# Optimization experiments

Measured on AMD Instinct MI355X. Metric: run time of the kernel, lower is better.

The kernel has to match this reference:

```python
import jax, jax.numpy as jnp
import numpy as np

B, S, D, H = 2, 2048, 1024, 16
HD = D // H  # head_dim = 64


def setup_inputs() -> dict:
    key = jax.random.key(0)
    ks = jax.random.split(key, 12)
    s = 1.0 / np.sqrt(D)
    return {
        "query": jax.random.normal(ks[0], (B, S, D), jnp.float32),
        "key": jax.random.normal(ks[1], (B, S, D), jnp.float32),
        "value": jax.random.normal(ks[2], (B, S, D), jnp.float32),
        "attention_mask": jnp.zeros((B, S, S), jnp.float32),
        "WQ_w": jax.random.normal(ks[3], (D, D), jnp.float32) * s,
        "WQ_b": jnp.zeros((D,), jnp.float32),
        "WK_w": jax.random.normal(ks[4], (D, D), jnp.float32) * s,
        "WK_b": jnp.zeros((D,), jnp.float32),
        "WV_w": jax.random.normal(ks[5], (D, D), jnp.float32) * s,
        "WV_b": jnp.zeros((D,), jnp.float32),
        "WO_w": jax.random.normal(ks[6], (D, D), jnp.float32) * s,
        "WO_b": jnp.zeros((D,), jnp.float32),
    }


def _split_heads(x):
    # [B,S,D] -> [B,H,S,HD]
    b, s, _ = x.shape
    return x.reshape(b, s, H, HD).transpose(0, 2, 1, 3)


def reference(query, key, value, attention_mask,
              WQ_w, WQ_b, WK_w, WK_b, WV_w, WV_b, WO_w, WO_b):
    Q = _split_heads(query @ WQ_w.T + WQ_b)   # [B,H,S,HD]
    K = _split_heads(key @ WK_w.T + WK_b)
    V = _split_heads(value @ WV_w.T + WV_b)
    scale = 1.0 / jnp.sqrt(jnp.float32(HD))
    scores = jnp.einsum('bhqd,bhkd->bhqk', Q, K) * scale
    scores = scores + attention_mask[:, None, :, :]
    attn = jax.nn.softmax(scores, axis=-1)    # dropout_prob=0.0 -> identity
    out = jnp.einsum('bhqk,bhkd->bhqd', attn, V)
    out = out.transpose(0, 2, 1, 3).reshape(query.shape[0], -1, D)
    return out @ WO_w.T + WO_b
```

## Files before the change

kernel.cpp:

```cpp
#include <hip/hip_runtime.h>
#include <math.h>


typedef _Float16 h8 __attribute__((ext_vector_type(8)));
typedef _Float16 h4 __attribute__((ext_vector_type(4)));
typedef float f4 __attribute__((ext_vector_type(4)));

#define MFMA16(a, b, c) __builtin_amdgcn_mfma_f32_16x16x32_f16((a), (b), (c), 0, 0, 0)
#define EXP2F(x) __builtin_amdgcn_exp2f(x)
#define BARRIER_LDS() asm volatile("s_waitcnt lgkmcnt(0)\n\ts_barrier" ::: "memory")

static constexpr int Bn = 2, Sn = 2048, Dn = 1024, Hn = 16, HDn = 64;
static constexpr int Mn = Bn * Sn;
static constexpr int Kn = Dn;
static constexpr int Nn = Dn;
static constexpr int LDP = 72;
static constexpr float LOG2E = 1.4426950408889634f;

__device__ __forceinline__ void gload_lds16(const _Float16* g, _Float16* l) {
  __builtin_amdgcn_global_load_lds(
      (const __attribute__((address_space(1))) unsigned int*)g,
      (__attribute__((address_space(3))) unsigned int*)l, 16, 0, 0);
}

struct CvtJobs {
  const float* src[8];
  _Float16* dst[8];
  int n4[8];
  float scl[8];
};

__global__ __launch_bounds__(256) void cvt_kernel(CvtJobs j) {
  const int stride = gridDim.x * blockDim.x;
  const int t0 = blockIdx.x * blockDim.x + threadIdx.x;
#pragma unroll
  for (int k = 0; k < 8; ++k) {
    const float4* __restrict__ s = (const float4*)j.src[k];
    h4* __restrict__ d = (h4*)j.dst[k];
    const int n = j.n4[k];
    const float sc = j.scl[k];
    for (int i = t0; i < n; i += stride) {
      const float4 f = s[i];
      h4 h;
      h[0] = (_Float16)(f.x * sc); h[1] = (_Float16)(f.y * sc);
      h[2] = (_Float16)(f.z * sc); h[3] = (_Float16)(f.w * sc);
      d[i] = h;
    }
  }
}

struct QkvArgs {
  const _Float16* X[3];
  const _Float16* W[3];
  const float* bias[3];
  _Float16* out[3];
};

__global__ __launch_bounds__(256) void gemm_qkv(QkvArgs args) {
  const int z = blockIdx.z;
  const _Float16* __restrict__ X = args.X[z];
  const _Float16* __restrict__ W = args.W[z];
  const float* __restrict__ bias = args.bias[z];
  _Float16* __restrict__ out = args.out[z];

  __shared__ _Float16 As[128 * 64];
  __shared__ _Float16 Bs[128 * 64];

  const int t = threadIdx.x;
  const int lane = t & 63, wv = t >> 6;
  const int l15 = lane & 15, quad = lane >> 4;
  const int wm = (wv >> 1) * 64, wn = (wv & 1) * 64;
  const int n0 = blockIdx.x * 128, m0 = blockIdx.y * 128;

  f4 acc[4][4];
#pragma unroll
  for (int i = 0; i < 4; ++i)
#pragma unroll
    for (int j = 0; j < 4; ++j) {
      f4 zz = {0.f, 0.f, 0.f, 0.f};
      acc[i][j] = zz;
    }

  const int srow = lane >> 3, scol = (lane & 7) * 8;

  for (int k0 = 0; k0 < Kn; k0 += 64) {
    __syncthreads();
#pragma unroll
    for (int u = 0; u < 4; ++u) {
      const int s = wv * 4 + u;
      const int row = s * 8 + srow;
      gload_lds16(X + (size_t)(m0 + row) * Kn + k0 + scol, As + s * 512);
      gload_lds16(W + (size_t)(n0 + row) * Kn + k0 + scol, Bs + s * 512);
    }
    __syncthreads();
#pragma unroll
    for (int kk = 0; kk < 64; kk += 32) {
      h8 af[4], bfr[4];
#pragma unroll
      for (int i = 0; i < 4; ++i)
        af[i] = *(const h8*)&As[(wm + i * 16 + l15) * 64 + kk + quad * 8];
#pragma unroll
      for (int j = 0; j < 4; ++j)
        bfr[j] = *(const h8*)&Bs[(wn + j * 16 + l15) * 64 + kk + quad * 8];
#pragma unroll
      for (int i = 0; i < 4; ++i)
#pragma unroll
        for (int j = 0; j < 4; ++j)
          acc[i][j] = MFMA16(af[i], bfr[j], acc[i][j]);
    }
  }

  const float osc = (z == 0) ? (0.125f * LOG2E) : 1.0f;
  if (z != 2) {
#pragma unroll
    for (int j = 0; j < 4; ++j) {
      const int n = n0 + wn + j * 16 + l15;
      const float bvs = bias[n] * osc;
      const int hh = n >> 6, hd = n & 63;
#pragma unroll
      for (int i = 0; i < 4; ++i) {
        const int mb = m0 + wm + i * 16 + quad * 4;
        const int bb = mb >> 11;
#pragma unroll
        for (int r = 0; r < 4; ++r) {
          const int ss = (mb + r) & (Sn - 1);
          out[(((size_t)(bb * Hn + hh)) * Sn + ss) * HDn + hd] =
              (_Float16)(acc[i][j][r] * osc + bvs);
        }
      }
    }
  } else {
#pragma unroll
    for (int j = 0; j < 4; ++j) {
      const int n = n0 + wn + j * 16 + l15;
      const float bv = bias[n];
      const int hh = n >> 6, hd = n & 63;
#pragma unroll
      for (int i = 0; i < 4; ++i) {
        const int mb = m0 + wm + i * 16 + quad * 4;
        const int bb = mb >> 11, ss = mb & (Sn - 1);
        h4 hv;
#pragma unroll
        for (int r = 0; r < 4; ++r) hv[r] = (_Float16)(acc[i][j][r] + bv);
        *(h4*)(out + (((size_t)(bb * Hn + hh)) * HDn + hd) * Sn + ss) = hv;
      }
    }
  }
}

__global__ __launch_bounds__(256) void gemm_o(const _Float16* __restrict__ X,
                                              const _Float16* __restrict__ W,
                                              const float* __restrict__ bias,
                                              float* __restrict__ out) {
  __shared__ _Float16 As[128 * 64];
  __shared__ _Float16 Bs[128 * 64];

  const int t = threadIdx.x;
  const int lane = t & 63, wv = t >> 6;
  const int l15 = lane & 15, quad = lane >> 4;
  const int wm = (wv >> 1) * 64, wn = (wv & 1) * 64;
  const int n0 = blockIdx.x * 128, m0 = blockIdx.y * 128;

  f4 acc[4][4];
#pragma unroll
  for (int i = 0; i < 4; ++i)
#pragma unroll
    for (int j = 0; j < 4; ++j) {
      f4 zz = {0.f, 0.f, 0.f, 0.f};
      acc[i][j] = zz;
    }

  const int srow = lane >> 3, scol = (lane & 7) * 8;

  for (int k0 = 0; k0 < Kn; k0 += 64) {
    __syncthreads();
#pragma unroll
    for (int u = 0; u < 4; ++u) {
      const int s = wv * 4 + u;
      const int row = s * 8 + srow;
      gload_lds16(X + (size_t)(m0 + row) * Kn + k0 + scol, As + s * 512);
      gload_lds16(W + (size_t)(n0 + row) * Kn + k0 + scol, Bs + s * 512);
    }
    __syncthreads();
#pragma unroll
    for (int kk = 0; kk < 64; kk += 32) {
      h8 af[4], bfr[4];
#pragma unroll
      for (int i = 0; i < 4; ++i)
        af[i] = *(const h8*)&As[(wm + i * 16 + l15) * 64 + kk + quad * 8];
#pragma unroll
      for (int j = 0; j < 4; ++j)
        bfr[j] = *(const h8*)&Bs[(wn + j * 16 + l15) * 64 + kk + quad * 8];
#pragma unroll
      for (int i = 0; i < 4; ++i)
#pragma unroll
        for (int j = 0; j < 4; ++j)
          acc[i][j] = MFMA16(af[i], bfr[j], acc[i][j]);
    }
  }

#pragma unroll
  for (int j = 0; j < 4; ++j) {
    const int n = n0 + wn + j * 16 + l15;
    const float bv = bias[n];
#pragma unroll
    for (int i = 0; i < 4; ++i) {
      const int mb = m0 + wm + i * 16 + quad * 4;
#pragma unroll
      for (int r = 0; r < 4; ++r)
        out[(size_t)(mb + r) * Nn + n] = acc[i][j][r] + bv;
    }
  }
}

__global__ __launch_bounds__(512) void attn_kernel(
    const _Float16* __restrict__ Qh,
    const _Float16* __restrict__ Kh,
    const _Float16* __restrict__ Vt,
    const _Float16* __restrict__ maskh,
    _Float16* __restrict__ out) {
  __shared__ _Float16 smem[4 * 64 * LDP];

  const int t = threadIdx.x;
  const int w = t >> 6, lane = t & 63;
  const int l15 = lane & 15, quad = lane >> 4;
  const int g = w >> 2;
  const int wq = w & 3;

  const int bh = blockIdx.y;
  const int b = bh >> 4, h = bh & 15;
  const size_t headoff = (size_t)bh * Sn * HDn;
  const _Float16* Qp = Qh + headoff;
  const _Float16* Kp = Kh + headoff;
  const _Float16* Vp = Vt + headoff;

  const int qb = blockIdx.x * 64;
  const int q0 = qb + wq * 16;
  const h8 qf0 = *(const h8*)(Qp + (size_t)(q0 + l15) * HDn + quad * 8);
  const h8 qf1 = *(const h8*)(Qp + (size_t)(q0 + l15) * HDn + 32 + quad * 8);

  const int kbase = g * (Sn / 2);
  const _Float16* mrow = maskh + ((size_t)b * Sn + q0 + l15) * Sn + kbase;

  float m_run = -INFINITY, l_part = 0.f;
  f4 o_acc[4];
#pragma unroll
  for (int nt = 0; nt < 4; ++nt) {
    f4 zz = {0.f, 0.f, 0.f, 0.f};
    o_acc[nt] = zz;
  }

  _Float16* Kg = smem + g * (64 * LDP);
  _Float16* Vg = smem + (2 + g) * (64 * LDP);

  const int tg = t & 255;
  const int srow = tg >> 3, sc8 = (tg & 7) * 8;
  const int srow1 = srow + 32;
  const int a = tg & 7;
  const int vb = ((a >> 2) & 1) * 32 + (a & 1) * 16 + ((a >> 1) & 1) * 4;

  constexpr int NT = (Sn / 2) / 64;

  uint4 kreg0, kreg1, vreg0, vreg1;
  uint2 mreg[4];
  auto kv_issue = [&](int kt) {
    kreg0 = *(const uint4*)(Kp + (size_t)(kbase + kt * 64 + srow) * HDn + sc8);
    vreg0 = *(const uint4*)(Vp + (size_t)srow * Sn + kbase + kt * 64 + sc8);
    kreg1 = *(const uint4*)(Kp + (size_t)(kbase + kt * 64 + srow1) * HDn + sc8);
    vreg1 = *(const uint4*)(Vp + (size_t)srow1 * Sn + kbase + kt * 64 + sc8);
  };
  auto m_issue = [&](int kt) {
#pragma unroll
    for (int ks = 0; ks < 4; ++ks)
      mreg[ks] = *(const uint2*)(mrow + kt * 64 + ks * 16 + quad * 4);
  };

  kv_issue(0);
  m_issue(0);

  for (int kt = 0; kt < NT; ++kt) {
    BARRIER_LDS();
    *(uint4*)&Kg[srow * LDP + sc8] = kreg0;
    *(uint4*)&Kg[srow1 * LDP + sc8] = kreg1;
    *(uint2*)&Vg[srow * LDP + vb] = make_uint2(vreg0.x, vreg0.y);
    *(uint2*)&Vg[srow * LDP + vb + 8] = make_uint2(vreg0.z, vreg0.w);
    *(uint2*)&Vg[srow1 * LDP + vb] = make_uint2(vreg1.x, vreg1.y);
    *(uint2*)&Vg[srow1 * LDP + vb + 8] = make_uint2(vreg1.z, vreg1.w);
    BARRIER_LDS();
    const int nx = (kt + 1 < NT) ? kt + 1 : kt;
    kv_issue(nx);

    f4 s[4];
#pragma unroll
    for (int ks = 0; ks < 4; ++ks) {
      const h4 mh = *(const h4*)&mreg[ks];
      f4 acc0;
#pragma unroll
      for (int r = 0; r < 4; ++r) acc0[r] = (float)mh[r];
      const h8 kf0 = *(const h8*)&Kg[(ks * 16 + l15) * LDP + quad * 8];
      const h8 kf1 = *(const h8*)&Kg[(ks * 16 + l15) * LDP + 32 + quad * 8];
      acc0 = MFMA16(kf0, qf0, acc0);
      s[ks] = MFMA16(kf1, qf1, acc0);
    }
    m_issue(nx);

    float mx = s[0][0];
#pragma unroll
    for (int ks = 0; ks < 4; ++ks)
#pragma unroll
      for (int r = 0; r < 4; ++r) mx = fmaxf(mx, s[ks][r]);
    mx = fmaxf(mx, __shfl_xor(mx, 16));
    mx = fmaxf(mx, __shfl_xor(mx, 32));
    if (!__all(mx - m_run <= 8.0f)) {
      const float nm = fmaxf(m_run, mx);
      const float alpha = EXP2F(m_run - nm);
      m_run = nm;
      l_part *= alpha;
#pragma unroll
      for (int nt = 0; nt < 4; ++nt)
#pragma unroll
        for (int r = 0; r < 4; ++r) o_acc[nt][r] *= alpha;
    }
    float sm = 0.f;
#pragma unroll
    for (int ks = 0; ks < 4; ++ks)
#pragma unroll
      for (int r = 0; r < 4; ++r) {
        s[ks][r] = EXP2F(s[ks][r] - m_run);
        sm += s[ks][r];
      }
    l_part += sm;

#pragma unroll
    for (int c = 0; c < 2; ++c) {
      h8 pf;
#pragma unroll
      for (int r = 0; r < 4; ++r) pf[r] = (_Float16)s[2 * c][r];
#pragma unroll
      for (int r = 0; r < 4; ++r) pf[4 + r] = (_Float16)s[2 * c + 1][r];
#pragma unroll
      for (int nt = 0; nt < 4; ++nt) {
        const h8 vf = *(const h8*)&Vg[(nt * 16 + l15) * LDP + c * 32 + quad * 8];
        o_acc[nt] = MFMA16(vf, pf, o_acc[nt]);
      }
    }
  }

  l_part += __shfl_xor(l_part, 16);
  l_part += __shfl_xor(l_part, 32);

  __syncthreads();
  float* Uex = (float*)smem;
  float* mex = Uex + 4 * 16 * LDP;
  float* lex = mex + 64;
  if (g == 1) {
#pragma unroll
    for (int nt = 0; nt < 4; ++nt)
      *(f4*)&Uex[wq * 16 * LDP + l15 * LDP + nt * 16 + quad * 4] = o_acc[nt];
    if (quad == 0) {
      mex[wq * 16 + l15] = m_run;
      lex[wq * 16 + l15] = l_part;
    }
  }
  __syncthreads();
  if (g == 0) {
    const float m1 = mex[wq * 16 + l15];
    const float l1 = lex[wq * 16 + l15];
    const float mm = fmaxf(m_run, m1);
    const float f0 = EXP2F(m_run - mm);
    const float f1 = EXP2F(m1 - mm);
    const float rl = 1.0f / (f0 * l_part + f1 * l1);
    _Float16* Ob = smem + 3 * (64 * LDP) + (w * 16) * LDP;
#pragma unroll
    for (int nt = 0; nt < 4; ++nt) {
      const f4 Ur = *(const f4*)&Uex[wq * 16 * LDP + l15 * LDP + nt * 16 + quad * 4];
      h4 ov;
#pragma unroll
      for (int r = 0; r < 4; ++r)
        ov[r] = (_Float16)((o_acc[nt][r] * f0 + Ur[r] * f1) * rl);
      *(h4*)&Ob[l15 * LDP + nt * 16 + quad * 4] = ov;
    }
    const int qr = lane >> 2;
    const int seg = (lane & 3) * 16;
    _Float16* dst = out + ((size_t)b * Sn + q0 + qr) * Dn + h * 64 + seg;
    *(uint4*)dst = *(const uint4*)&Ob[qr * LDP + seg];
    *(uint4*)(dst + 8) = *(const uint4*)&Ob[qr * LDP + seg + 8];
  }
}

extern "C" void kernel_launch(void* const* d_in, const int* in_sizes, int n_in,
                              void* d_out, int out_size, void* d_ws, size_t ws_size,
                              hipStream_t stream) {
  const float* q = (const float*)d_in[0];
  const float* k = (const float*)d_in[1];
  const float* v = (const float*)d_in[2];
  const float* mask = (const float*)d_in[3];
  const float* WQ = (const float*)d_in[4];
  const float* bQ = (const float*)d_in[5];
  const float* WK = (const float*)d_in[6];
  const float* bK = (const float*)d_in[7];
  const float* WV = (const float*)d_in[8];
  const float* bV = (const float*)d_in[9];
  const float* WO = (const float*)d_in[10];
  const float* bO = (const float*)d_in[11];

  _Float16* ws = (_Float16*)d_ws;
  const size_t MD = (size_t)Mn * Dn;
  const size_t DD = (size_t)Dn * Dn;
  const size_t SS = (size_t)Bn * Sn * Sn;
  _Float16* qh  = ws;
  _Float16* kh  = ws + MD;
  _Float16* vh  = ws + 2 * MD;
  _Float16* WQh = ws + 3 * MD;
  _Float16* WKh = WQh + DD;
  _Float16* WVh = WKh + DD;
  _Float16* WOh = WVh + DD;
  _Float16* Qh  = ws + 3 * MD + 4 * DD;
  _Float16* Kh  = Qh + MD;
  _Float16* Vt  = Kh + MD;
  _Float16* AO  = qh;
  const size_t used = 6 * MD + 4 * DD;
  _Float16* Mh = (ws_size >= (used + SS) * sizeof(_Float16))
                     ? (ws + used)
                     : (_Float16*)d_out;

  CvtJobs cj;
  cj.src[0] = q;    cj.dst[0] = qh;  cj.n4[0] = (int)(MD / 4);  cj.scl[0] = 1.f;
  cj.src[1] = k;    cj.dst[1] = kh;  cj.n4[1] = (int)(MD / 4);  cj.scl[1] = 1.f;
  cj.src[2] = v;    cj.dst[2] = vh;  cj.n4[2] = (int)(MD / 4);  cj.scl[2] = 1.f;
  cj.src[3] = WQ;   cj.dst[3] = WQh; cj.n4[3] = (int)(DD / 4);  cj.scl[3] = 1.f;
  cj.src[4] = WK;   cj.dst[4] = WKh; cj.n4[4] = (int)(DD / 4);  cj.scl[4] = 1.f;
  cj.src[5] = WV;   cj.dst[5] = WVh; cj.n4[5] = (int)(DD / 4);  cj.scl[5] = 1.f;
  cj.src[6] = WO;   cj.dst[6] = WOh; cj.n4[6] = (int)(DD / 4);  cj.scl[6] = 1.f;
  cj.src[7] = mask; cj.dst[7] = Mh;  cj.n4[7] = (int)(SS / 4);  cj.scl[7] = LOG2E;
  cvt_kernel<<<1024, 256, 0, stream>>>(cj);

  QkvArgs ga;
  ga.X[0] = qh; ga.W[0] = WQh; ga.bias[0] = bQ; ga.out[0] = Qh;
  ga.X[1] = kh; ga.W[1] = WKh; ga.bias[1] = bK; ga.out[1] = Kh;
  ga.X[2] = vh; ga.W[2] = WVh; ga.bias[2] = bV; ga.out[2] = Vt;
  gemm_qkv<<<dim3(Nn / 128, Mn / 128, 3), 256, 0, stream>>>(ga);

  attn_kernel<<<dim3(Sn / 64, Bn * Hn), 512, 0, stream>>>(Qh, Kh, Vt, Mh, AO);

  gemm_o<<<dim3(Nn / 128, Mn / 128), 256, 0, stream>>>(AO, WOh, bO, (float*)d_out);
}
```

Before: 301.5 us.

## Double-buffer LDS tiles in QKV and output projection GEMMs

Both projection GEMMs now keep two LDS buffers per operand and issue the async global-to-LDS loads for the next K tile before computing on the current one. A single vmcnt(0) wait plus barrier per iteration replaces the two __syncthreads. The goal is to hide global load latency behind the MFMA work. LDS use per block doubles to 64 KB, which may reduce how many blocks fit on a CU. Correctness also depends on the vmcnt wait covering the LDS-direct loads before the buffer is read.

```diff
diff --git a/kernel.cpp b/kernel.cpp
--- a/kernel.cpp
+++ b/kernel.cpp
@@ -9,6 +9,9 @@
 #define MFMA16(a, b, c) __builtin_amdgcn_mfma_f32_16x16x32_f16((a), (b), (c), 0, 0, 0)
 #define EXP2F(x) __builtin_amdgcn_exp2f(x)
 #define BARRIER_LDS() asm volatile("s_waitcnt lgkmcnt(0)\n\ts_barrier" ::: "memory")
+#define BARRIER_VM0() do { \
+  asm volatile("s_waitcnt vmcnt(0)" ::: "memory"); \
+  __builtin_amdgcn_s_barrier(); } while (0)
 
 static constexpr int Bn = 2, Sn = 2048, Dn = 1024, Hn = 16, HDn = 64;
 static constexpr int Mn = Bn * Sn;
@@ -63,8 +66,8 @@
   const float* __restrict__ bias = args.bias[z];
   _Float16* __restrict__ out = args.out[z];
 
-  __shared__ _Float16 As[128 * 64];
-  __shared__ _Float16 Bs[128 * 64];
+  __shared__ _Float16 As[2][128 * 64];
+  __shared__ _Float16 Bs[2][128 * 64];
 
   const int t = threadIdx.x;
   const int lane = t & 63, wv = t >> 6;
@@ -83,31 +86,39 @@
 
   const int srow = lane >> 3, scol = (lane & 7) * 8;
 
-  for (int k0 = 0; k0 < Kn; k0 += 64) {
-    __syncthreads();
+  auto stage = [&](int buf, int k0) {
 #pragma unroll
     for (int u = 0; u < 4; ++u) {
       const int s = wv * 4 + u;
       const int row = s * 8 + srow;
-      gload_lds16(X + (size_t)(m0 + row) * Kn + k0 + scol, As + s * 512);
-      gload_lds16(W + (size_t)(n0 + row) * Kn + k0 + scol, Bs + s * 512);
-    }
-    __syncthreads();
+      gload_lds16(X + (size_t)(m0 + row) * Kn + k0 + scol, &As[buf][s * 512]);
+      gload_lds16(W + (size_t)(n0 + row) * Kn + k0 + scol, &Bs[buf][s * 512]);
+    }
+  };
+
+  stage(0, 0);
+  BARRIER_VM0();
+
+  constexpr int NKT = Kn / 64;
+  for (int kt = 0; kt < NKT; ++kt) {
+    const int cur = kt & 1;
+    if (kt + 1 < NKT) stage(cur ^ 1, (kt + 1) * 64);
 #pragma unroll
     for (int kk = 0; kk < 64; kk += 32) {
       h8 af[4], bfr[4];
 #pragma unroll
       for (int i = 0; i < 4; ++i)
-        af[i] = *(const h8*)&As[(wm + i * 16 + l15) * 64 + kk + quad * 8];
+        af[i] = *(const h8*)&As[cur][(wm + i * 16 + l15) * 64 + kk + quad * 8];
 #pragma unroll
       for (int j = 0; j < 4; ++j)
-        bfr[j] = *(const h8*)&Bs[(wn + j * 16 + l15) * 64 + kk + quad * 8];
+        bfr[j] = *(const h8*)&Bs[cur][(wn + j * 16 + l15) * 64 + kk + quad * 8];
 #pragma unroll
       for (int i = 0; i < 4; ++i)
 #pragma unroll
         for (int j = 0; j < 4; ++j)
           acc[i][j] = MFMA16(af[i], bfr[j], acc[i][j]);
     }
+    BARRIER_VM0();
   }
 
   const float osc = (z == 0) ? (0.125f * LOG2E) : 1.0f;
@@ -152,8 +163,8 @@
                                               const _Float16* __restrict__ W,
                                               const float* __restrict__ bias,
                                               float* __restrict__ out) {
-  __shared__ _Float16 As[128 * 64];
-  __shared__ _Float16 Bs[128 * 64];
+  __shared__ _Float16 As[2][128 * 64];
+  __shared__ _Float16 Bs[2][128 * 64];
 
   const int t = threadIdx.x;
   const int lane = t & 63, wv = t >> 6;
@@ -172,31 +183,39 @@
 
   const int srow = lane >> 3, scol = (lane & 7) * 8;
 
-  for (int k0 = 0; k0 < Kn; k0 += 64) {
-    __syncthreads();
+  auto stage = [&](int buf, int k0) {
 #pragma unroll
     for (int u = 0; u < 4; ++u) {
       const int s = wv * 4 + u;
       const int row = s * 8 + srow;
-      gload_lds16(X + (size_t)(m0 + row) * Kn + k0 + scol, As + s * 512);
-      gload_lds16(W + (size_t)(n0 + row) * Kn + k0 + scol, Bs + s * 512);
-    }
-    __syncthreads();
+      gload_lds16(X + (size_t)(m0 + row) * Kn + k0 + scol, &As[buf][s * 512]);
+      gload_lds16(W + (size_t)(n0 + row) * Kn + k0 + scol, &Bs[buf][s * 512]);
+    }
+  };
+
+  stage(0, 0);
+  BARRIER_VM0();
+
+  constexpr int NKT = Kn / 64;
+  for (int kt = 0; kt < NKT; ++kt) {
+    const int cur = kt & 1;
+    if (kt + 1 < NKT) stage(cur ^ 1, (kt + 1) * 64);
 #pragma unroll
     for (int kk = 0; kk < 64; kk += 32) {
       h8 af[4], bfr[4];
 #pragma unroll
       for (int i = 0; i < 4; ++i)
-        af[i] = *(const h8*)&As[(wm + i * 16 + l15) * 64 + kk + quad * 8];
+        af[i] = *(const h8*)&As[cur][(wm + i * 16 + l15) * 64 + kk + quad * 8];
 #pragma unroll
       for (int j = 0; j < 4; ++j)
-        bfr[j] = *(const h8*)&Bs[(wn + j * 16 + l15) * 64 + kk + quad * 8];
+        bfr[j] = *(const h8*)&Bs[cur][(wn + j * 16 + l15) * 64 + kk + quad * 8];
 #pragma unroll
       for (int i = 0; i < 4; ++i)
 #pragma unroll
         for (int j = 0; j < 4; ++j)
           acc[i][j] = MFMA16(af[i], bfr[j], acc[i][j]);
     }
+    BARRIER_VM0();
   }
 
 #pragma unroll
```

After: 321.0 us. 6.5% more time.
